# Kernel tuning notes

Hardware: AMD Instinct MI355X
Metric: run time of the kernel (lower is better)

## Reference

```python
import jax, jax.numpy as jnp
import numpy as np

THRESHOLD = 0.8
SECONDARY = 0.5
SECONDARY_WEIGHT = 0.5
N_PATCH = 196  # 14*14 patches of 2x2 pixels from a 28x28 image


def setup_inputs() -> dict:
    key = jax.random.key(0)
    k = jax.random.split(key, 5)
    B = 4096
    x = jax.random.uniform(k[0], (B, 1, 28, 28), dtype=jnp.float32)
    W1 = jax.random.normal(k[1], (4, 32), dtype=jnp.float32) * 0.5
    b1 = jnp.zeros((32,), jnp.float32)
    W2 = jax.random.normal(k[2], (32, 10), dtype=jnp.float32) * 0.2
    b2 = jnp.zeros((10,), jnp.float32)
    return {"x": x, "W1": W1, "b1": b1, "W2": W2, "b2": b2}


def _forward(x, W1, b1, W2, b2):
    B = x.shape[0]
    img = x[:, 0]  # (B, 28, 28)
    # extract 2x2 stride-2 patches -> (B, 196, 4), pixel order (0,0),(0,1),(1,0),(1,1)
    patches = img.reshape(B, 14, 2, 14, 2).transpose(0, 1, 3, 2, 4).reshape(B, N_PATCH, 4)
    # quantum patch encoder surrogate: PauliZ expectation after RY(theta) encoding is cos(theta)
    q = jnp.cos(patches)  # (B, 196, 4)
    # pairwise state fidelity = squared cosine similarity, via one batched matmul
    qn = q / (jnp.linalg.norm(q, axis=-1, keepdims=True) + 1e-12)
    fid = jnp.einsum('bnd,bmd->bnm', qn, qn) ** 2  # (B, 196, 196)
    # threshold-edge adjacency: 1.0 above threshold, secondary_weight in [secondary, threshold)
    adj = jnp.where(fid >= THRESHOLD, 1.0,
                    jnp.where(fid >= SECONDARY, SECONDARY_WEIGHT, 0.0))
    adj = jnp.where(jnp.eye(N_PATCH, dtype=bool), 0.0, adj)  # no self-edges (u<v pairs only)
    # GraphAggregation pools over all 196 nodes (all nodes are added to the graph)
    pooled = jnp.mean(q, axis=1)  # (B, 4)
    logits = (pooled @ W1 + b1) @ W2 + b2  # (B, 10)
    return logits, adj


def reference(x, W1, b1, W2, b2):
    return _forward(x, W1, b1, W2, b2)
```

## Files before the change

### kernel.cpp

```cpp
#include <hip/hip_runtime.h>
#include <math.h>


#define NP   196
#define NPIX 784
#define BLK  256
#define NV   (NP * NP / 4)
#define VPR  (NP / 4)

typedef float f32x4 __attribute__((ext_vector_type(4)));

__global__ __launch_bounds__(BLK) void quanv_kernel(
    const float* __restrict__ x,
    const float* __restrict__ W1, const float* __restrict__ b1,
    const float* __restrict__ W2, const float* __restrict__ b2,
    float* __restrict__ logits, float* __restrict__ adj)
{
    __shared__ float q4[NP][4];
    __shared__ __align__(16) float qnT[4][NP];
    __shared__ float pooled[4];

    const int b   = blockIdx.x;
    const int tid = threadIdx.x;
    const float* img = x + (size_t)b * NPIX;

    for (int p = tid; p < NPIX; p += BLK) {
        int r = p / 28;
        int c = p - r * 28;
        int n  = (r >> 1) * 14 + (c >> 1);
        int dd = ((r & 1) << 1) | (c & 1);
        q4[n][dd] = cosf(img[p]);
    }
    __syncthreads();

    if (tid < NP) {
        float a0 = q4[tid][0], a1 = q4[tid][1], a2 = q4[tid][2], a3 = q4[tid][3];
        float nrm = sqrtf(a0*a0 + a1*a1 + a2*a2 + a3*a3);
        float inv = 1.0f / (nrm + 1e-12f);
        qnT[0][tid] = a0 * inv;
        qnT[1][tid] = a1 * inv;
        qnT[2][tid] = a2 * inv;
        qnT[3][tid] = a3 * inv;
    }

    if (tid < 64) {
        float s0 = 0.f, s1 = 0.f, s2 = 0.f, s3 = 0.f;
        for (int n = tid; n < NP; n += 64) {
            s0 += q4[n][0]; s1 += q4[n][1]; s2 += q4[n][2]; s3 += q4[n][3];
        }
        #pragma unroll
        for (int off = 32; off >= 1; off >>= 1) {
            s0 += __shfl_down(s0, off);
            s1 += __shfl_down(s1, off);
            s2 += __shfl_down(s2, off);
            s3 += __shfl_down(s3, off);
        }
        if (tid == 0) {
            pooled[0] = s0 * (1.0f / NP);
            pooled[1] = s1 * (1.0f / NP);
            pooled[2] = s2 * (1.0f / NP);
            pooled[3] = s3 * (1.0f / NP);
        }
    }
    __syncthreads();

    if (tid < 10) {
        float p0 = pooled[0], p1 = pooled[1], p2 = pooled[2], p3 = pooled[3];
        float acc = b2[tid];
        #pragma unroll
        for (int k = 0; k < 32; ++k) {
            float h = b1[k] + p0 * W1[0*32 + k] + p1 * W1[1*32 + k]
                            + p2 * W1[2*32 + k] + p3 * W1[3*32 + k];
            acc += h * W2[k*10 + tid];
        }
        logits[(size_t)b * 10 + tid] = acc;
    }

    f32x4* out4 = reinterpret_cast<f32x4*>(adj + (size_t)b * (NP * NP));
    for (int e4 = tid; e4 < NV; e4 += BLK) {
        int n  = e4 / VPR;
        int m0 = (e4 - n * VPR) * 4;

        float c0 = qnT[0][n], c1 = qnT[1][n], c2 = qnT[2][n], c3 = qnT[3][n];
        f32x4 v0 = *reinterpret_cast<const f32x4*>(&qnT[0][m0]);
        f32x4 v1 = *reinterpret_cast<const f32x4*>(&qnT[1][m0]);
        f32x4 v2 = *reinterpret_cast<const f32x4*>(&qnT[2][m0]);
        f32x4 v3 = *reinterpret_cast<const f32x4*>(&qnT[3][m0]);

        f32x4 d = c0*v0 + c1*v1 + c2*v2 + c3*v3;
        f32x4 f = d * d;

        f32x4 o;
        o.x = (f.x >= 0.8f) ? 1.0f : ((f.x >= 0.5f) ? 0.5f : 0.0f);
        o.y = (f.y >= 0.8f) ? 1.0f : ((f.y >= 0.5f) ? 0.5f : 0.0f);
        o.z = (f.z >= 0.8f) ? 1.0f : ((f.z >= 0.5f) ? 0.5f : 0.0f);
        o.w = (f.w >= 0.8f) ? 1.0f : ((f.w >= 0.5f) ? 0.5f : 0.0f);

        if (n >= m0 && n < m0 + 4) {
            if      (n == m0)     o.x = 0.0f;
            else if (n == m0 + 1) o.y = 0.0f;
            else if (n == m0 + 2) o.z = 0.0f;
            else                  o.w = 0.0f;
        }
        out4[e4] = o;
    }
}

extern "C" void kernel_launch(void* const* d_in, const int* in_sizes, int n_in,
                              void* d_out, int out_size, void* d_ws, size_t ws_size,
                              hipStream_t stream) {
    const float* x  = (const float*)d_in[0];
    const float* W1 = (const float*)d_in[1];
    const float* b1 = (const float*)d_in[2];
    const float* W2 = (const float*)d_in[3];
    const float* b2 = (const float*)d_in[4];

    const int B = in_sizes[0] / NPIX;
    float* logits = (float*)d_out;
    float* adj    = logits + (size_t)B * 10;

    quanv_kernel<<<B, BLK, 0, stream>>>(x, W1, b1, W2, b2, logits, adj);
}
```

Before: 150.3 us.

## Restructure adjacency loop with per-lane column registers and nontemporal stores

Switches the normalized patch layout to row-major and assigns each wave a quarter of the rows. Each lane keeps four column vectors in registers and iterates over rows, removing the per-element integer division and most LDS loads. Output stores become nontemporal to avoid polluting cache. Only 49 of 64 lanes are active per wave, which may reduce store issue efficiency.

```diff
diff --git a/kernel.cpp b/kernel.cpp
--- a/kernel.cpp
+++ b/kernel.cpp
@@ -5,7 +5,6 @@
 #define NP   196
 #define NPIX 784
 #define BLK  256
-#define NV   (NP * NP / 4)
 #define VPR  (NP / 4)
 
 typedef float f32x4 __attribute__((ext_vector_type(4)));
@@ -17,11 +16,13 @@
     float* __restrict__ logits, float* __restrict__ adj)
 {
     __shared__ float q4[NP][4];
-    __shared__ __align__(16) float qnT[4][NP];
+    __shared__ __align__(16) float qnA[NP][4];
     __shared__ float pooled[4];
 
     const int b   = blockIdx.x;
     const int tid = threadIdx.x;
+    const int w   = tid >> 6;
+    const int l   = tid & 63;
     const float* img = x + (size_t)b * NPIX;
 
     for (int p = tid; p < NPIX; p += BLK) {
@@ -35,12 +36,11 @@
 
     if (tid < NP) {
         float a0 = q4[tid][0], a1 = q4[tid][1], a2 = q4[tid][2], a3 = q4[tid][3];
-        float nrm = sqrtf(a0*a0 + a1*a1 + a2*a2 + a3*a3);
-        float inv = 1.0f / (nrm + 1e-12f);
-        qnT[0][tid] = a0 * inv;
-        qnT[1][tid] = a1 * inv;
-        qnT[2][tid] = a2 * inv;
-        qnT[3][tid] = a3 * inv;
+        float inv = 1.0f / (sqrtf(a0*a0 + a1*a1 + a2*a2 + a3*a3) + 1e-12f);
+        qnA[tid][0] = a0 * inv;
+        qnA[tid][1] = a1 * inv;
+        qnA[tid][2] = a2 * inv;
+        qnA[tid][3] = a3 * inv;
     }
 
     if (tid < 64) {
@@ -76,33 +76,37 @@
         logits[(size_t)b * 10 + tid] = acc;
     }
 
-    f32x4* out4 = reinterpret_cast<f32x4*>(adj + (size_t)b * (NP * NP));
-    for (int e4 = tid; e4 < NV; e4 += BLK) {
-        int n  = e4 / VPR;
-        int m0 = (e4 - n * VPR) * 4;
+    if (l < VPR) {
+        const f32x4 p0 = *reinterpret_cast<const f32x4*>(&qnA[4*l + 0][0]);
+        const f32x4 p1 = *reinterpret_cast<const f32x4*>(&qnA[4*l + 1][0]);
+        const f32x4 p2 = *reinterpret_cast<const f32x4*>(&qnA[4*l + 2][0]);
+        const f32x4 p3 = *reinterpret_cast<const f32x4*>(&qnA[4*l + 3][0]);
+        const int col0 = 4*l;
 
-        float c0 = qnT[0][n], c1 = qnT[1][n], c2 = qnT[2][n], c3 = qnT[3][n];
-        f32x4 v0 = *reinterpret_cast<const f32x4*>(&qnT[0][m0]);
-        f32x4 v1 = *reinterpret_cast<const f32x4*>(&qnT[1][m0]);
-        f32x4 v2 = *reinterpret_cast<const f32x4*>(&qnT[2][m0]);
-        f32x4 v3 = *reinterpret_cast<const f32x4*>(&qnT[3][m0]);
+        f32x4* outb = reinterpret_cast<f32x4*>(adj + (size_t)b * (NP * NP));
+        const int nEnd = VPR * (w + 1);
+        for (int n = VPR * w; n < nEnd; ++n) {
+            f32x4 c = *reinterpret_cast<const f32x4*>(&qnA[n][0]);
+            f32x4 d;
+            d.x = c.x*p0.x + c.y*p0.y + c.z*p0.z + c.w*p0.w;
+            d.y = c.x*p1.x + c.y*p1.y + c.z*p1.z + c.w*p1.w;
+            d.z = c.x*p2.x + c.y*p2.y + c.z*p2.z + c.w*p2.w;
+            d.w = c.x*p3.x + c.y*p3.y + c.z*p3.z + c.w*p3.w;
+            f32x4 f = d * d;
 
-        f32x4 d = c0*v0 + c1*v1 + c2*v2 + c3*v3;
-        f32x4 f = d * d;
+            f32x4 o;
+            o.x = (f.x >= 0.8f) ? 1.0f : ((f.x >= 0.5f) ? 0.5f : 0.0f);
+            o.y = (f.y >= 0.8f) ? 1.0f : ((f.y >= 0.5f) ? 0.5f : 0.0f);
+            o.z = (f.z >= 0.8f) ? 1.0f : ((f.z >= 0.5f) ? 0.5f : 0.0f);
+            o.w = (f.w >= 0.8f) ? 1.0f : ((f.w >= 0.5f) ? 0.5f : 0.0f);
 
-        f32x4 o;
-        o.x = (f.x >= 0.8f) ? 1.0f : ((f.x >= 0.5f) ? 0.5f : 0.0f);
-        o.y = (f.y >= 0.8f) ? 1.0f : ((f.y >= 0.5f) ? 0.5f : 0.0f);
-        o.z = (f.z >= 0.8f) ? 1.0f : ((f.z >= 0.5f) ? 0.5f : 0.0f);
-        o.w = (f.w >= 0.8f) ? 1.0f : ((f.w >= 0.5f) ? 0.5f : 0.0f);
+            o.x = (col0 + 0 == n) ? 0.0f : o.x;
+            o.y = (col0 + 1 == n) ? 0.0f : o.y;
+            o.z = (col0 + 2 == n) ? 0.0f : o.z;
+            o.w = (col0 + 3 == n) ? 0.0f : o.w;
 
-        if (n >= m0 && n < m0 + 4) {
-            if      (n == m0)     o.x = 0.0f;
-            else if (n == m0 + 1) o.y = 0.0f;
-            else if (n == m0 + 2) o.z = 0.0f;
-            else                  o.w = 0.0f;
+            __builtin_nontemporal_store(o, &outb[n * VPR + l]);
         }
-        out4[e4] = o;
     }
 }
 
```

New measurement: 178.9 us. +19.1%, slower.
